# Performance work log

Hardware: AMD Instinct MI355X
Metric: run time of the kernel (lower is better)

Reference implementation:

```python
import jax, jax.numpy as jnp
import numpy as np

B, T, C = 4, 2048, 1024
H = 16
HD = C // H  # 64


def setup_inputs() -> dict:
    key = jax.random.key(0)
    k1, k2, k3 = jax.random.split(key, 3)
    x = jax.random.normal(k1, (B, T, C), dtype=jnp.float32)
    W_attn = jax.random.normal(k2, (C, 3 * C), dtype=jnp.float32) * (1.0 / np.sqrt(C))
    b_attn = jnp.zeros((3 * C,), dtype=jnp.float32)
    W_proj = jax.random.normal(k3, (C, C), dtype=jnp.float32) * (1.0 / np.sqrt(C))
    b_proj = jnp.zeros((C,), dtype=jnp.float32)
    return {"x": x, "W_attn": W_attn, "b_attn": b_attn, "W_proj": W_proj, "b_proj": b_proj}


def reference(x, W_attn, b_attn, W_proj, b_proj):
    Bx, Tx, Cx = x.shape
    qkv = x @ W_attn + b_attn                      # [B,T,3C]
    q, k, v = jnp.split(qkv, 3, axis=-1)
    # [B,T,C] -> [B,H,T,HD]
    q = q.reshape(Bx, Tx, H, HD).transpose(0, 2, 1, 3)
    k = k.reshape(Bx, Tx, H, HD).transpose(0, 2, 1, 3)
    v = v.reshape(Bx, Tx, H, HD).transpose(0, 2, 1, 3)
    att = jnp.einsum('bhqd,bhkd->bhqk', q, k) / jnp.sqrt(jnp.float32(HD))
    causal = jnp.tril(jnp.ones((Tx, Tx), dtype=bool))
    att = jnp.where(causal[None, None], att, -jnp.inf)
    att = jax.nn.softmax(att, axis=-1)
    y = jnp.einsum('bhqk,bhkd->bhqd', att, v)      # [B,H,T,HD]
    y = y.transpose(0, 2, 1, 3).reshape(Bx, Tx, Cx)
    return y @ W_proj + b_proj
```

## Files before the change

kernel.cpp:

```cpp
#include <hip/hip_runtime.h>
#include <hip/hip_bf16.h>

typedef unsigned short u16;
typedef __attribute__((ext_vector_type(8))) short bf16x8;
typedef __attribute__((ext_vector_type(4))) float f32x4;

#define MFMA16(a, b, c) __builtin_amdgcn_mfma_f32_16x16x32_bf16((a), (b), (c), 0, 0, 0)

__device__ __forceinline__ u16 f2bf(float f) {
  union { float f; unsigned u; } v; v.f = f;
  unsigned r = v.u + 0x7fffu + ((v.u >> 16) & 1u);
  return (u16)(r >> 16);
}

__device__ __forceinline__ unsigned pk_trunc(float hi, float lo) {
  union { float f; unsigned u; } a, b; a.f = hi; b.f = lo;
  return __builtin_amdgcn_perm(a.u, b.u, 0x07060302u);
}

__device__ __forceinline__ void gload_lds16(const u16* g, u16* l) {
  __builtin_amdgcn_global_load_lds((const __attribute__((address_space(1))) void*)g,
                                   (__attribute__((address_space(3))) void*)l, 16, 0, 0);
}

__global__ __launch_bounds__(256) void convert_bf16_k(const float* __restrict__ in,
                                                      u16* __restrict__ out, int n) {
  int i = (blockIdx.x * 256 + threadIdx.x) * 8;
  if (i >= n) return;
  float4 v0 = *(const float4*)(in + i);
  float4 v1 = *(const float4*)(in + i + 4);
  uint4 o;
  o.x = (unsigned)f2bf(v0.x) | ((unsigned)f2bf(v0.y) << 16);
  o.y = (unsigned)f2bf(v0.z) | ((unsigned)f2bf(v0.w) << 16);
  o.z = (unsigned)f2bf(v1.x) | ((unsigned)f2bf(v1.y) << 16);
  o.w = (unsigned)f2bf(v1.z) | ((unsigned)f2bf(v1.w) << 16);
  *(uint4*)(out + i) = o;
}

__global__ __launch_bounds__(256) void transpose2_k(const float* __restrict__ Wa, u16* __restrict__ WaT,
                                                    const float* __restrict__ Wp, u16* __restrict__ WpT) {
  __shared__ float tile[64][65];
  int b = blockIdx.x;
  const float* W; u16* Wt; int N, n0, k0;
  if (b < 768) { W = Wa; Wt = WaT; N = 3072; n0 = (b % 48) * 64; k0 = (b / 48) * 64; }
  else { int c = b - 768; W = Wp; Wt = WpT; N = 1024; n0 = (c & 15) * 64; k0 = (c >> 4) * 64; }
  const int tx = threadIdx.x & 63, ty = threadIdx.x >> 6;
#pragma unroll
  for (int i = 0; i < 16; ++i)
    tile[ty + 4 * i][tx] = W[(size_t)(k0 + ty + 4 * i) * N + n0 + tx];
  __syncthreads();
#pragma unroll
  for (int i = 0; i < 16; ++i)
    Wt[(size_t)(n0 + ty + 4 * i) * 1024 + k0 + tx] = f2bf(tile[tx][ty + 4 * i]);
}

#define BAR() asm volatile("s_barrier" ::: "memory")
#define WLG()                                                   \
  do {                                                          \
    asm volatile("s_waitcnt lgkmcnt(0)" ::: "memory");          \
    __builtin_amdgcn_sched_barrier(0);                          \
  } while (0)
#define VMW0() asm volatile("s_waitcnt vmcnt(0)" ::: "memory")

#define LANE_CONSTS                                                       \
  const int tid = threadIdx.x, w = tid >> 6, lane = tid & 63;             \
  const int wm = w >> 2, wn = w & 3;                                      \
  const int fr = lane & 15, fg = lane >> 4;                               \
  const int sr = lane >> 2;                                               \
  const int sk = (lane & 1) * 8 + ((((lane >> 1) ^ (lane >> 5)) & 1) << 4); \
  const int kc = (w & 1) * 32 + sk;                                       \
  const int r0g = (w >> 1) * 16 + sr;                                     \
  const int lsw = fr * 32 + ((fg * 8) ^ ((fr & 8) ? 16 : 0));

__global__ __launch_bounds__(512, 2) void gemm_qkv_8p(const u16* __restrict__ A,
                                                      const u16* __restrict__ Bt,
                                                      const float* __restrict__ bias,
                                                      u16* __restrict__ Qo, u16* __restrict__ Ko,
                                                      u16* __restrict__ Vt) {
  __shared__ u16 sm[2][32768];
  const int bid = blockIdx.x;
  const int swz = (bid & 7) * 48 + (bid >> 3);
  const int m0 = (swz / 12) * 256, n0 = (swz % 12) * 256;
  LANE_CONSTS
  const int aoff = wm * 8192 + lsw;
  const int boff = 16384 + (wn >> 1) * 8192 + (wn & 1) * 4096 + lsw;

  const u16* gA = A + (size_t)(m0 + r0g) * 1024 + kc;
  const u16* gB = Bt + (size_t)(n0 + r0g) * 1024 + kc;

#define QSTGA(D, H, C) \
  gload_lds16(gA + (size_t)(H) * 131072 + (C) * 65536, &sm[(D)][(H) * 8192 + (C) * 4096 + w * 512])
#define QSTGB(D, H, C) \
  gload_lds16(gB + (size_t)(H) * 131072 + (C) * 65536, &sm[(D)][16384 + (H) * 8192 + (C) * 4096 + w * 512])

  f32x4 acc[8][4];
#pragma unroll
  for (int i = 0; i < 8; ++i)
#pragma unroll
    for (int j = 0; j < 4; ++j) acc[i][j] = (f32x4){0, 0, 0, 0};

  QSTGA(0, 0, 0); QSTGA(0, 0, 1); QSTGA(0, 1, 0); QSTGA(0, 1, 1);
  QSTGB(0, 0, 0); QSTGB(0, 0, 1); QSTGB(0, 1, 0); QSTGB(0, 1, 1);
  gA += 64; gB += 64;
  VMW0(); BAR();

#define QLDA(B_, KK, M0_)                                                 \
  _Pragma("unroll") for (int i = 0; i < 4; ++i)                           \
      av[i] = *(const bf16x8*)&sm[(B_)][aoff + (((M0_) + i) * 2 + (KK)) * 512];
#define QLDB(B_, KK)                                                      \
  _Pragma("unroll") for (int i = 0; i < 4; ++i)                           \
      bv[i] = *(const bf16x8*)&sm[(B_)][boff + (i * 2 + (KK)) * 512];
#define QMM(MB0)                                                          \
  __builtin_amdgcn_s_setprio(1);                                          \
  _Pragma("unroll") for (int i = 0; i < 4; ++i)                           \
      _Pragma("unroll") for (int j = 0; j < 4; ++j)                       \
          acc[(MB0) + i][j] = MFMA16(av[i], bv[j], acc[(MB0) + i][j]);    \
  __builtin_amdgcn_s_setprio(0);

#define QTILE(B_, S_)                                                          \
  {                                                                            \
    bf16x8 av[4], bv[4];                                                       \
                       \
    QLDA(B_, 0, 0) QLDB(B_, 0)                                                 \
    if (S_) { QSTGA((B_) ^ 1, 0, 0); QSTGA((B_) ^ 1, 0, 1);                    \
              QSTGA((B_) ^ 1, 1, 0); QSTGA((B_) ^ 1, 1, 1); }                  \
    BAR(); WLG(); QMM(0) BAR();                                                \
                               \
    QLDA(B_, 0, 4)                                                             \
    if (S_) { QSTGB((B_) ^ 1, 0, 0); QSTGB((B_) ^ 1, 0, 1);                    \
              QSTGB((B_) ^ 1, 1, 0); QSTGB((B_) ^ 1, 1, 1); }                  \
    BAR(); WLG(); QMM(4) BAR();                                                \
                                                  \
    QLDA(B_, 1, 0) QLDB(B_, 1)                                                 \
    BAR(); WLG(); QMM(0) BAR();                                                \
                       \
    QLDA(B_, 1, 4)                                                             \
    BAR(); WLG(); QMM(4)                                                       \
    if (S_) { VMW0(); gA += 64; gB += 64; }                                    \
    BAR();                                                                     \
  }

#pragma unroll 1
  for (int tp = 0; tp < 7; ++tp) { QTILE(0, 1) QTILE(1, 1) }
  QTILE(0, 1)
  QTILE(1, 0)

  const int which = n0 >> 10;
#pragma unroll
  for (int nb = 0; nb < 4; ++nb) {
    const int n = n0 + wn * 64 + nb * 16 + fr;
    const float bs = bias[n];
    const int c = n & 1023, h = c >> 6, hd = c & 63;
#pragma unroll
    for (int mb = 0; mb < 8; ++mb) {
      const int mbase = m0 + wm * 128 + mb * 16 + fg * 4;
      const int bb = mbase >> 11;
      const int tt = mbase & 2047;
      if (which == 0) {
        u16* dst = Qo + ((size_t)(bb * 16 + h) * 2048 + tt) * 64 + hd;
#pragma unroll
        for (int r = 0; r < 4; ++r) dst[(size_t)r * 64] = f2bf((acc[mb][nb][r] + bs) * 0.125f);
      } else if (which == 1) {
        u16* dst = Ko + ((size_t)(bb * 16 + h) * 2048 + tt) * 64 + hd;
#pragma unroll
        for (int r = 0; r < 4; ++r) dst[(size_t)r * 64] = f2bf(acc[mb][nb][r] + bs);
      } else {
        ushort4 pv;
        pv.x = f2bf(acc[mb][nb][0] + bs);
        pv.y = f2bf(acc[mb][nb][1] + bs);
        pv.z = f2bf(acc[mb][nb][2] + bs);
        pv.w = f2bf(acc[mb][nb][3] + bs);
        *(ushort4*)(Vt + ((size_t)(bb * 16 + h) * 64 + hd) * 2048 + tt) = pv;
      }
    }
  }
#undef QSTGA
#undef QSTGB
#undef QLDA
#undef QLDB
#undef QMM
#undef QTILE
}

__global__ __launch_bounds__(512, 2) void gemm_proj_8p(const u16* __restrict__ A,
                                                       const u16* __restrict__ Bt,
                                                       const float* __restrict__ bias,
                                                       float* __restrict__ O) {
  __shared__ u16 sm[2][24576];
  const int bid = blockIdx.x;
  const int swz = (bid & 7) * 32 + (bid >> 3);
  const int m0 = (swz >> 3) * 256, n0 = (swz & 7) * 128;
  LANE_CONSTS
  const int aoff = wm * 8192 + lsw;
  const int boff = 16384 + wn * 2048 + lsw;

  const u16* gA = A + (size_t)(m0 + r0g) * 1024 + kc;
  const u16* gB = Bt + (size_t)(n0 + r0g) * 1024 + kc;

#define PSTGA(D, H, C) \
  gload_lds16(gA + (size_t)(H) * 131072 + (C) * 65536, &sm[(D)][(H) * 8192 + (C) * 4096 + w * 512])
#define PSTGB(D, C) \
  gload_lds16(gB + (size_t)(C) * 65536, &sm[(D)][16384 + (C) * 4096 + w * 512])

  f32x4 acc[8][2];
#pragma unroll
  for (int i = 0; i < 8; ++i)
#pragma unroll
    for (int j = 0; j < 2; ++j) acc[i][j] = (f32x4){0, 0, 0, 0};

  PSTGA(0, 0, 0); PSTGA(0, 0, 1); PSTGA(0, 1, 0); PSTGA(0, 1, 1);
  PSTGB(0, 0); PSTGB(0, 1);
  gA += 64; gB += 64;
  VMW0(); BAR();

#define PLDA(B_, KK, M0_)                                                 \
  _Pragma("unroll") for (int i = 0; i < 4; ++i)                           \
      av[i] = *(const bf16x8*)&sm[(B_)][aoff + (((M0_) + i) * 2 + (KK)) * 512];
#define PLDB(B_, KK)                                                      \
  _Pragma("unroll") for (int i = 0; i < 2; ++i)                           \
      bv[i] = *(const bf16x8*)&sm[(B_)][boff + (i * 2 + (KK)) * 512];
#define PMM(MB0)                                                          \
  __builtin_amdgcn_s_setprio(1);                                          \
  _Pragma("unroll") for (int i = 0; i < 4; ++i)                           \
      _Pragma("unroll") for (int j = 0; j < 2; ++j)                       \
          acc[(MB0) + i][j] = MFMA16(av[i], bv[j], acc[(MB0) + i][j]);    \
  __builtin_amdgcn_s_setprio(0);

#define PTILE(B_, S_)                                                          \
  {                                                                            \
    bf16x8 av[4], bv[2];                                                       \
    PLDA(B_, 0, 0) PLDB(B_, 0)                                                 \
    if (S_) { PSTGA((B_) ^ 1, 0, 0); PSTGA((B_) ^ 1, 0, 1);                    \
              PSTGA((B_) ^ 1, 1, 0); PSTGA((B_) ^ 1, 1, 1); }                  \
    BAR(); WLG(); PMM(0) BAR();                                                \
    PLDA(B_, 0, 4)                                                             \
    if (S_) { PSTGB((B_) ^ 1, 0); PSTGB((B_) ^ 1, 1); }                        \
    BAR(); WLG(); PMM(4) BAR();                                                \
    PLDA(B_, 1, 0) PLDB(B_, 1)                                                 \
    BAR(); WLG(); PMM(0) BAR();                                                \
    PLDA(B_, 1, 4)                                                             \
    BAR(); WLG(); PMM(4)                                                       \
    if (S_) { VMW0(); gA += 64; gB += 64; }                                    \
    BAR();                                                                     \
  }

#pragma unroll 1
  for (int tp = 0; tp < 7; ++tp) { PTILE(0, 1) PTILE(1, 1) }
  PTILE(0, 1)
  PTILE(1, 0)

#pragma unroll
  for (int nb = 0; nb < 2; ++nb) {
    const int n = n0 + wn * 32 + nb * 16 + fr;
    const float bs = bias[n];
#pragma unroll
    for (int mb = 0; mb < 8; ++mb) {
      const int tg = m0 + wm * 128 + mb * 16 + fg * 4;
#pragma unroll
      for (int r = 0; r < 4; ++r) O[(size_t)(tg + r) * 1024 + n] = acc[mb][nb][r] + bs;
    }
  }
#undef PSTGA
#undef PSTGB
#undef PLDA
#undef PLDB
#undef PMM
#undef PTILE
}

#define PSTR 72
__global__ __launch_bounds__(256) void attn_k(const u16* __restrict__ Q,
                                              const u16* __restrict__ Kb,
                                              const u16* __restrict__ Vt,
                                              u16* __restrict__ Y) {
  __shared__ u16 Ks[64 * 72];
  __shared__ u16 Vs[64 * 72];
  __shared__ u16 Ps[4 * 32 * PSTR];
  const int L = blockIdx.x;
  const int xcd = L & 7, slot = L >> 3;
  const int bh = xcd * 8 + (slot & 7);
  const int qt = 15 - (slot >> 3);
  const int tid = threadIdx.x, w = tid >> 6, lane = tid & 63;
  const int fr = lane & 15, fg = lane >> 4;
  const u16* Qp = Q + (size_t)bh * 2048 * 64;
  const u16* Kp = Kb + (size_t)bh * 2048 * 64;
  const u16* Vp = Vt + (size_t)bh * 64 * 2048;
  const int qw = qt * 128 + w * 32;

  bf16x8 qa[2][2];
#pragma unroll
  for (int g = 0; g < 2; ++g)
#pragma unroll
    for (int c = 0; c < 2; ++c)
      qa[g][c] = *(const bf16x8*)(Qp + (size_t)(qw + g * 16 + fr) * 64 + c * 32 + fg * 8);

  float li[2] = {0.f, 0.f};
  f32x4 ot[2][4];
#pragma unroll
  for (int g = 0; g < 2; ++g)
#pragma unroll
    for (int mb = 0; mb < 4; ++mb) ot[g][mb] = (f32x4){0, 0, 0, 0};

  const int srow = tid >> 2, scol = (tid & 3) * 16;
  u16* Pw = Ps + w * 32 * PSTR;
  const int nk = 2 * qt + 2;
  const u16* Kg = Kp + (size_t)srow * 64 + scol;
  const u16* Vg = Vp + (size_t)srow * 2048 + scol;

  uint4 kr0 = *(const uint4*)(Kg);
  uint4 kr1 = *(const uint4*)(Kg + 8);
  uint4 vr0 = *(const uint4*)(Vg);
  uint4 vr1 = *(const uint4*)(Vg + 8);

  for (int jt = 0; jt < nk; ++jt) {
    const int k0 = jt * 64;
    if (jt) __syncthreads();
    *(uint4*)&Ks[srow * 72 + scol] = kr0;
    *(uint4*)&Ks[srow * 72 + scol + 8] = kr1;
    *(uint4*)&Vs[srow * 72 + scol] = vr0;
    *(uint4*)&Vs[srow * 72 + scol + 8] = vr1;
    __syncthreads();
    if (jt + 1 < nk) {
      const int kn = (jt + 1) * 64;
      kr0 = *(const uint4*)(Kg + (size_t)kn * 64);
      kr1 = *(const uint4*)(Kg + (size_t)kn * 64 + 8);
      vr0 = *(const uint4*)(Vg + kn);
      vr1 = *(const uint4*)(Vg + kn + 8);
    }
    if (k0 > qw + 31) continue;

    bf16x8 kb[4][2];
#pragma unroll
    for (int nb = 0; nb < 4; ++nb) {
      kb[nb][0] = *(const bf16x8*)&Ks[(nb * 16 + fr) * 72 + fg * 8];
      kb[nb][1] = *(const bf16x8*)&Ks[(nb * 16 + fr) * 72 + 32 + fg * 8];
    }
    f32x4 st[2][4];
#pragma unroll
    for (int g = 0; g < 2; ++g)
#pragma unroll
      for (int nb = 0; nb < 4; ++nb) {
        f32x4 z = (f32x4){0, 0, 0, 0};
        z = MFMA16(kb[nb][0], qa[g][0], z);
        z = MFMA16(kb[nb][1], qa[g][1], z);
        st[g][nb] = z;
      }
    const bool needmask = (k0 + 63 > qw);
#pragma unroll
    for (int g = 0; g < 2; ++g) {
      const int q = qw + g * 16 + fr;
      float rs0 = 0.f, rs1 = 0.f;
#pragma unroll
      for (int nb = 0; nb < 4; ++nb) {
        const int kcb = k0 + nb * 16 + 4 * fg;
        float p0 = __expf(st[g][nb][0]);
        float p1 = __expf(st[g][nb][1]);
        float p2 = __expf(st[g][nb][2]);
        float p3 = __expf(st[g][nb][3]);
        if (needmask) {
          p0 = (kcb + 0 > q) ? 0.f : p0;
          p1 = (kcb + 1 > q) ? 0.f : p1;
          p2 = (kcb + 2 > q) ? 0.f : p2;
          p3 = (kcb + 3 > q) ? 0.f : p3;
        }
        rs0 += p0 + p1;
        rs1 += p2 + p3;
        *(uint2*)&Pw[(g * 16 + fr) * PSTR + nb * 16 + 4 * fg] =
            make_uint2(pk_trunc(p1, p0), pk_trunc(p3, p2));
      }
      li[g] += rs0 + rs1;
    }
    bf16x8 pa[2][2];
#pragma unroll
    for (int g = 0; g < 2; ++g)
#pragma unroll
      for (int H = 0; H < 2; ++H)
        pa[g][H] = *(const bf16x8*)&Pw[(g * 16 + fr) * PSTR + H * 32 + fg * 8];
#pragma unroll
    for (int mb = 0; mb < 4; ++mb) {
      bf16x8 vb0 = *(const bf16x8*)&Vs[(mb * 16 + fr) * 72 + fg * 8];
      bf16x8 vb1 = *(const bf16x8*)&Vs[(mb * 16 + fr) * 72 + 32 + fg * 8];
#pragma unroll
      for (int g = 0; g < 2; ++g) {
        ot[g][mb] = MFMA16(vb0, pa[g][0], ot[g][mb]);
        ot[g][mb] = MFMA16(vb1, pa[g][1], ot[g][mb]);
      }
    }
  }

  const int b = bh >> 4, h = bh & 15;
#pragma unroll
  for (int g = 0; g < 2; ++g) {
    float l = li[g];
    l += __shfl_xor(l, 16);
    l += __shfl_xor(l, 32);
    const float inv = 1.0f / l;
    const int t = qw + g * 16 + fr;
    u16* yrow = Y + ((size_t)b * 2048 + t) * 1024 + h * 64;
#pragma unroll
    for (int mb = 0; mb < 4; ++mb) {
      const unsigned d0 = (unsigned)f2bf(ot[g][mb][0] * inv) |
                          ((unsigned)f2bf(ot[g][mb][1] * inv) << 16);
      const unsigned d1 = (unsigned)f2bf(ot[g][mb][2] * inv) |
                          ((unsigned)f2bf(ot[g][mb][3] * inv) << 16);
      *(uint2*)&yrow[mb * 16 + fg * 4] = make_uint2(d0, d1);
    }
  }
}

extern "C" void kernel_launch(void* const* d_in, const int* in_sizes, int n_in,
                              void* d_out, int out_size, void* d_ws, size_t ws_size,
                              hipStream_t stream) {
  const float* x = (const float*)d_in[0];
  const float* Wa = (const float*)d_in[1];
  const float* ba = (const float*)d_in[2];
  const float* Wp = (const float*)d_in[3];
  const float* bp = (const float*)d_in[4];
  float* out = (float*)d_out;

  char* p = (char*)d_ws;
  u16* xb = (u16*)p;   p += (size_t)8192 * 1024 * 2;
  u16* WaT = (u16*)p;  p += (size_t)3072 * 1024 * 2;
  u16* WpT = (u16*)p;  p += (size_t)1024 * 1024 * 2;
  u16* Qb = (u16*)p;   p += (size_t)64 * 2048 * 64 * 2;
  u16* Kbuf = (u16*)p; p += (size_t)64 * 2048 * 64 * 2;
  u16* Vtb = (u16*)p;  p += (size_t)64 * 64 * 2048 * 2;
  u16* Yb = (u16*)p;   p += (size_t)8192 * 1024 * 2;

  convert_bf16_k<<<4096, 256, 0, stream>>>(x, xb, 8192 * 1024);
  transpose2_k<<<1024, 256, 0, stream>>>(Wa, WaT, Wp, WpT);
  gemm_qkv_8p<<<384, 512, 0, stream>>>(xb, WaT, ba, Qb, Kbuf, Vtb);
  attn_k<<<1024, 256, 0, stream>>>(Qb, Kbuf, Vtb, Yb);
  gemm_proj_8p<<<256, 512, 0, stream>>>(Yb, WpT, bp, out);
}
```

Measured before the change: 254.3 us.

## Replace double-buffered K=64 GEMM staging with 4-slot K=32 ring buffers

```diff
diff --git a/kernel.cpp b/kernel.cpp
--- a/kernel.cpp
+++ b/kernel.cpp
@@ -60,38 +60,36 @@
     asm volatile("s_waitcnt lgkmcnt(0)" ::: "memory");          \
     __builtin_amdgcn_sched_barrier(0);                          \
   } while (0)
-#define VMW0() asm volatile("s_waitcnt vmcnt(0)" ::: "memory")
-
-#define LANE_CONSTS                                                       \
-  const int tid = threadIdx.x, w = tid >> 6, lane = tid & 63;             \
-  const int wm = w >> 2, wn = w & 3;                                      \
-  const int fr = lane & 15, fg = lane >> 4;                               \
-  const int sr = lane >> 2;                                               \
+#define VMW(N) asm volatile("s_waitcnt vmcnt(" #N ")" ::: "memory")
+
+#define RING_LANE_CONSTS                                                    \
+  const int tid = threadIdx.x, w = tid >> 6, lane = tid & 63;               \
+  const int wm = w >> 2, wn = w & 3;                                        \
+  const int fr = lane & 15, fg = lane >> 4;                                 \
+  const int sr = lane >> 2;                                                 \
   const int sk = (lane & 1) * 8 + ((((lane >> 1) ^ (lane >> 5)) & 1) << 4); \
-  const int kc = (w & 1) * 32 + sk;                                       \
-  const int r0g = (w >> 1) * 16 + sr;                                     \
   const int lsw = fr * 32 + ((fg * 8) ^ ((fr & 8) ? 16 : 0));
 
-__global__ __launch_bounds__(512, 2) void gemm_qkv_8p(const u16* __restrict__ A,
+__global__ __launch_bounds__(512, 2) void gemm_qkv_r4(const u16* __restrict__ A,
                                                       const u16* __restrict__ Bt,
                                                       const float* __restrict__ bias,
                                                       u16* __restrict__ Qo, u16* __restrict__ Ko,
                                                       u16* __restrict__ Vt) {
-  __shared__ u16 sm[2][32768];
+  __shared__ u16 sm[4][16384];
   const int bid = blockIdx.x;
   const int swz = (bid & 7) * 48 + (bid >> 3);
   const int m0 = (swz / 12) * 256, n0 = (swz % 12) * 256;
-  LANE_CONSTS
-  const int aoff = wm * 8192 + lsw;
-  const int boff = 16384 + (wn >> 1) * 8192 + (wn & 1) * 4096 + lsw;
-
-  const u16* gA = A + (size_t)(m0 + r0g) * 1024 + kc;
-  const u16* gB = Bt + (size_t)(n0 + r0g) * 1024 + kc;
-
-#define QSTGA(D, H, C) \
-  gload_lds16(gA + (size_t)(H) * 131072 + (C) * 65536, &sm[(D)][(H) * 8192 + (C) * 4096 + w * 512])
-#define QSTGB(D, H, C) \
-  gload_lds16(gB + (size_t)(H) * 131072 + (C) * 65536, &sm[(D)][16384 + (H) * 8192 + (C) * 4096 + w * 512])
+  RING_LANE_CONSTS
+  const int aoff = wm * 4096 + lsw;
+  const int boff = 8192 + wn * 2048 + lsw;
+
+  const u16* gAw = A + (size_t)(m0 + sr) * 1024 + sk + (size_t)w * 16384;
+  const u16* gBw = Bt + (size_t)(n0 + sr) * 1024 + sk + (size_t)w * 16384;
+
+#define QSTG_A(SL, C, KO) \
+  gload_lds16(gAw + (size_t)(C) * 131072 + (KO), &sm[SL][(C) * 4096 + w * 512 + lane * 8])
+#define QSTG_B(SL, C, KO) \
+  gload_lds16(gBw + (size_t)(C) * 131072 + (KO), &sm[SL][8192 + (C) * 4096 + w * 512 + lane * 8])
 
   f32x4 acc[8][4];
 #pragma unroll
@@ -99,17 +97,18 @@
 #pragma unroll
     for (int j = 0; j < 4; ++j) acc[i][j] = (f32x4){0, 0, 0, 0};
 
-  QSTGA(0, 0, 0); QSTGA(0, 0, 1); QSTGA(0, 1, 0); QSTGA(0, 1, 1);
-  QSTGB(0, 0, 0); QSTGB(0, 0, 1); QSTGB(0, 1, 0); QSTGB(0, 1, 1);
-  gA += 64; gB += 64;
-  VMW0(); BAR();
-
-#define QLDA(B_, KK, M0_)                                                 \
+  QSTG_A(0, 0, 0);  QSTG_B(0, 0, 0);  QSTG_A(0, 1, 0);  QSTG_B(0, 1, 0);
+  QSTG_A(1, 0, 32); QSTG_B(1, 0, 32); QSTG_A(1, 1, 32); QSTG_B(1, 1, 32);
+  QSTG_A(2, 0, 64); QSTG_B(2, 0, 64); QSTG_A(2, 1, 64); QSTG_B(2, 1, 64);
+  int kofs = 96;
+  VMW(8); BAR();
+
+#define QLD_A(SL, M0_)                                                    \
   _Pragma("unroll") for (int i = 0; i < 4; ++i)                           \
-      av[i] = *(const bf16x8*)&sm[(B_)][aoff + (((M0_) + i) * 2 + (KK)) * 512];
-#define QLDB(B_, KK)                                                      \
+      av[i] = *(const bf16x8*)&sm[SL][aoff + ((M0_) + i) * 512];
+#define QLD_B(SL)                                                         \
   _Pragma("unroll") for (int i = 0; i < 4; ++i)                           \
-      bv[i] = *(const bf16x8*)&sm[(B_)][boff + (i * 2 + (KK)) * 512];
+      bv[i] = *(const bf16x8*)&sm[SL][boff + i * 512];
 #define QMM(MB0)                                                          \
   __builtin_amdgcn_s_setprio(1);                                          \
   _Pragma("unroll") for (int i = 0; i < 4; ++i)                           \
@@ -117,33 +116,28 @@
           acc[(MB0) + i][j] = MFMA16(av[i], bv[j], acc[(MB0) + i][j]);    \
   __builtin_amdgcn_s_setprio(0);
 
-#define QTILE(B_, S_)                                                          \
+#define QTILE(SL, SS, STG, CHK)                                                \
   {                                                                            \
     bf16x8 av[4], bv[4];                                                       \
-                       \
-    QLDA(B_, 0, 0) QLDB(B_, 0)                                                 \
-    if (S_) { QSTGA((B_) ^ 1, 0, 0); QSTGA((B_) ^ 1, 0, 1);                    \
-              QSTGA((B_) ^ 1, 1, 0); QSTGA((B_) ^ 1, 1, 1); }                  \
+    QLD_A(SL, 0) QLD_B(SL)                                                     \
+    if (STG) { QSTG_A(SS, 0, kofs); QSTG_B(SS, 0, kofs); }                     \
     BAR(); WLG(); QMM(0) BAR();                                                \
-                               \
-    QLDA(B_, 0, 4)                                                             \
-    if (S_) { QSTGB((B_) ^ 1, 0, 0); QSTGB((B_) ^ 1, 0, 1);                    \
-              QSTGB((B_) ^ 1, 1, 0); QSTGB((B_) ^ 1, 1, 1); }                  \
-    BAR(); WLG(); QMM(4) BAR();                                                \
-                                                  \
-    QLDA(B_, 1, 0) QLDB(B_, 1)                                                 \
-    BAR(); WLG(); QMM(0) BAR();                                                \
-                       \
-    QLDA(B_, 1, 4)                                                             \
+    QLD_A(SL, 4)                                                               \
+    if (STG) { QSTG_A(SS, 1, kofs); QSTG_B(SS, 1, kofs); }                     \
     BAR(); WLG(); QMM(4)                                                       \
-    if (S_) { VMW0(); gA += 64; gB += 64; }                                    \
+    CHK;                                                                       \
     BAR();                                                                     \
+    kofs += 32;                                                                \
   }
 
 #pragma unroll 1
-  for (int tp = 0; tp < 7; ++tp) { QTILE(0, 1) QTILE(1, 1) }
-  QTILE(0, 1)
-  QTILE(1, 0)
+  for (int tp = 0; tp < 7; ++tp) {
+    QTILE(0, 3, 1, VMW(8)) QTILE(1, 0, 1, VMW(8)) QTILE(2, 1, 1, VMW(8)) QTILE(3, 2, 1, VMW(8))
+  }
+  QTILE(0, 3, 1, VMW(8))
+  QTILE(1, 0, 0, VMW(4))
+  QTILE(2, 0, 0, VMW(0))
+  QTILE(3, 0, 0, (void)0)
 
   const int which = n0 >> 10;
 #pragma unroll
@@ -174,33 +168,33 @@
       }
     }
   }
-#undef QSTGA
-#undef QSTGB
-#undef QLDA
-#undef QLDB
+#undef QSTG_A
+#undef QSTG_B
+#undef QLD_A
+#undef QLD_B
 #undef QMM
 #undef QTILE
 }
 
-__global__ __launch_bounds__(512, 2) void gemm_proj_8p(const u16* __restrict__ A,
+__global__ __launch_bounds__(512, 2) void gemm_proj_r4(const u16* __restrict__ A,
                                                        const u16* __restrict__ Bt,
                                                        const float* __restrict__ bias,
                                                        float* __restrict__ O) {
-  __shared__ u16 sm[2][24576];
+  __shared__ u16 sm[4][12288];
   const int bid = blockIdx.x;
   const int swz = (bid & 7) * 32 + (bid >> 3);
   const int m0 = (swz >> 3) * 256, n0 = (swz & 7) * 128;
-  LANE_CONSTS
-  const int aoff = wm * 8192 + lsw;
-  const int boff = 16384 + wn * 2048 + lsw;
-
-  const u16* gA = A + (size_t)(m0 + r0g) * 1024 + kc;
-  const u16* gB = Bt + (size_t)(n0 + r0g) * 1024 + kc;
-
-#define PSTGA(D, H, C) \
-  gload_lds16(gA + (size_t)(H) * 131072 + (C) * 65536, &sm[(D)][(H) * 8192 + (C) * 4096 + w * 512])
-#define PSTGB(D, C) \
-  gload_lds16(gB + (size_t)(C) * 65536, &sm[(D)][16384 + (C) * 4096 + w * 512])
+  RING_LANE_CONSTS
+  const int aoff = wm * 4096 + lsw;
+  const int boff = 8192 + wn * 1024 + lsw;
+
+  const u16* gAw = A + (size_t)(m0 + sr) * 1024 + sk + (size_t)w * 16384;
+  const u16* gBw = Bt + (size_t)(n0 + sr) * 1024 + sk + (size_t)w * 16384;
+
+#define PSTG_A(SL, C, KO) \
+  gload_lds16(gAw + (size_t)(C) * 131072 + (KO), &sm[SL][(C) * 4096 + w * 512 + lane * 8])
+#define PSTG_B(SL, KO) \
+  gload_lds16(gBw + (KO), &sm[SL][8192 + w * 512 + lane * 8])
 
   f32x4 acc[8][2];
 #pragma unroll
@@ -208,17 +202,18 @@
 #pragma unroll
     for (int j = 0; j < 2; ++j) acc[i][j] = (f32x4){0, 0, 0, 0};
 
-  PSTGA(0, 0, 0); PSTGA(0, 0, 1); PSTGA(0, 1, 0); PSTGA(0, 1, 1);
-  PSTGB(0, 0); PSTGB(0, 1);
-  gA += 64; gB += 64;
-  VMW0(); BAR();
-
-#define PLDA(B_, KK, M0_)                                                 \
+  PSTG_A(0, 0, 0);  PSTG_B(0, 0);  PSTG_A(0, 1, 0);
+  PSTG_A(1, 0, 32); PSTG_B(1, 32); PSTG_A(1, 1, 32);
+  PSTG_A(2, 0, 64); PSTG_B(2, 64); PSTG_A(2, 1, 64);
+  int kofs = 96;
+  VMW(6); BAR();
+
+#define PLD_A(SL, M0_)                                                    \
   _Pragma("unroll") for (int i = 0; i < 4; ++i)                           \
-      av[i] = *(const bf16x8*)&sm[(B_)][aoff + (((M0_) + i) * 2 + (KK)) * 512];
-#define PLDB(B_, KK)                                                      \
+      av[i] = *(const bf16x8*)&sm[SL][aoff + ((M0_) + i) * 512];
+#define PLD_B(SL)                                                         \
   _Pragma("unroll") for (int i = 0; i < 2; ++i)                           \
-      bv[i] = *(const bf16x8*)&sm[(B_)][boff + (i * 2 + (KK)) * 512];
+      bv[i] = *(const bf16x8*)&sm[SL][boff + i * 512];
 #define PMM(MB0)                                                          \
   __builtin_amdgcn_s_setprio(1);                                          \
   _Pragma("unroll") for (int i = 0; i < 4; ++i)                           \
@@ -226,28 +221,28 @@
           acc[(MB0) + i][j] = MFMA16(av[i], bv[j], acc[(MB0) + i][j]);    \
   __builtin_amdgcn_s_setprio(0);
 
-#define PTILE(B_, S_)                                                          \
+#define PTILE(SL, SS, STG, CHK)                                                \
   {                                                                            \
     bf16x8 av[4], bv[2];                                                       \
-    PLDA(B_, 0, 0) PLDB(B_, 0)                                                 \
-    if (S_) { PSTGA((B_) ^ 1, 0, 0); PSTGA((B_) ^ 1, 0, 1);                    \
-              PSTGA((B_) ^ 1, 1, 0); PSTGA((B_) ^ 1, 1, 1); }                  \
+    PLD_A(SL, 0) PLD_B(SL)                                                     \
+    if (STG) { PSTG_A(SS, 0, kofs); PSTG_B(SS, kofs); }                        \
     BAR(); WLG(); PMM(0) BAR();                                                \
-    PLDA(B_, 0, 4)                                                             \
-    if (S_) { PSTGB((B_) ^ 1, 0); PSTGB((B_) ^ 1, 1); }                        \
-    BAR(); WLG(); PMM(4) BAR();                                                \
-    PLDA(B_, 1, 0) PLDB(B_, 1)                                                 \
-    BAR(); WLG(); PMM(0) BAR();                                                \
-    PLDA(B_, 1, 4)                                                             \
+    PLD_A(SL, 4)                                                               \
+    if (STG) { PSTG_A(SS, 1, kofs); }                                          \
     BAR(); WLG(); PMM(4)                                                       \
-    if (S_) { VMW0(); gA += 64; gB += 64; }                                    \
+    CHK;                                                                       \
     BAR();                                                                     \
+    kofs += 32;                                                                \
   }
 
 #pragma unroll 1
-  for (int tp = 0; tp < 7; ++tp) { PTILE(0, 1) PTILE(1, 1) }
-  PTILE(0, 1)
-  PTILE(1, 0)
+  for (int tp = 0; tp < 7; ++tp) {
+    PTILE(0, 3, 1, VMW(6)) PTILE(1, 0, 1, VMW(6)) PTILE(2, 1, 1, VMW(6)) PTILE(3, 2, 1, VMW(6))
+  }
+  PTILE(0, 3, 1, VMW(6))
+  PTILE(1, 0, 0, VMW(3))
+  PTILE(2, 0, 0, VMW(0))
+  PTILE(3, 0, 0, (void)0)
 
 #pragma unroll
   for (int nb = 0; nb < 2; ++nb) {
@@ -260,10 +255,10 @@
       for (int r = 0; r < 4; ++r) O[(size_t)(tg + r) * 1024 + n] = acc[mb][nb][r] + bs;
     }
   }
-#undef PSTGA
-#undef PSTGB
-#undef PLDA
-#undef PLDB
+#undef PSTG_A
+#undef PSTG_B
+#undef PLD_A
+#undef PLD_B
 #undef PMM
 #undef PTILE
 }
@@ -429,7 +424,7 @@
 
   convert_bf16_k<<<4096, 256, 0, stream>>>(x, xb, 8192 * 1024);
   transpose2_k<<<1024, 256, 0, stream>>>(Wa, WaT, Wp, WpT);
-  gemm_qkv_8p<<<384, 512, 0, stream>>>(xb, WaT, ba, Qb, Kbuf, Vtb);
+  gemm_qkv_r4<<<384, 512, 0, stream>>>(xb, WaT, ba, Qb, Kbuf, Vtb);
   attn_k<<<1024, 256, 0, stream>>>(Qb, Kbuf, Vtb, Yb);
-  gemm_proj_8p<<<256, 512, 0, stream>>>(Yb, WpT, bp, out);
-}
+  gemm_proj_r4<<<256, 512, 0, stream>>>(Yb, WpT, bp, out);
+}
```

New measurement: 250.9 us. Within noise of the previous version (-1.3%).
